# Performance work log

Hardware: AMD Instinct MI355X
Metric: run time of the kernel (lower is better)

Reference implementation:

```python
import jax, jax.numpy as jnp
import numpy as np

N = 4096


def setup_inputs() -> dict:
    key = jax.random.key(0)
    ks = jax.random.split(key, 5)
    s = 1.0 / np.sqrt(N)  # PyTorch Linear default init scale
    return {
        "outer": jax.random.normal(ks[0], (N, N), dtype=jnp.float32),
        "W_slice": jax.random.uniform(ks[1], (N, N), jnp.float32, -s, s),
        "b_slice": jax.random.uniform(ks[2], (N,), jnp.float32, -s, s),
        "W_q": jax.random.uniform(ks[3], (N, N), jnp.float32, -s, s),
        "b_q": jax.random.uniform(ks[4], (N,), jnp.float32, -s, s),
    }


def reference(outer, W_slice, b_slice, W_q, b_q):
    # k = sigmoid(Linear(outer)) then transposed: [n, n] -> [n, n]
    k = jax.nn.sigmoid(outer @ W_slice.T + b_slice).T
    # q = sigmoid(Linear(outer)): [n, n]
    q = jax.nn.sigmoid(outer @ W_q.T + b_q)
    # elementwise score, softmax over last dim (legacy nn.Softmax dim=1 for 2D)
    attn = jax.nn.softmax(q * k, axis=1)
    # weighted sum then reduce: [n, n] @ [n, n] -> [n, n] -> sum(-1) -> [n]
    out = (attn @ outer).sum(-1)
    return out
```

## Files before the change

### kernel.cpp

```cpp
#include <hip/hip_runtime.h>
#include <hip/hip_bf16.h>
#include <hip/hip_fp16.h>

#define NN 4096

typedef __attribute__((ext_vector_type(8))) __bf16 bf16x8;
typedef __attribute__((ext_vector_type(4))) float f32x4;
typedef __attribute__((ext_vector_type(8))) _Float16 f16x8;

static __device__ __forceinline__ unsigned short f2bf_bits(float x) {
  __hip_bfloat16 h = __float2bfloat16(x);
  return __builtin_bit_cast(unsigned short, h);
}

__global__ __launch_bounds__(256) void cast_rowsum_kernel(
    const float* __restrict__ in, __hip_bfloat16* __restrict__ ob,
    float* __restrict__ s) {
  const int row = blockIdx.x;
  const int t = threadIdx.x;
  const float4* rp = (const float4*)(in + (size_t)row * NN);
  unsigned short* op = (unsigned short*)(ob + (size_t)row * NN);
  float sum = 0.f;
#pragma unroll
  for (int it = 0; it < 4; ++it) {
    const int idx = it * 256 + t;
    float4 v = rp[idx];
    sum += (v.x + v.y) + (v.z + v.w);
    ushort4 b;
    b.x = f2bf_bits(v.x);
    b.y = f2bf_bits(v.y);
    b.z = f2bf_bits(v.z);
    b.w = f2bf_bits(v.w);
    *(ushort4*)(op + idx * 4) = b;
  }
#pragma unroll
  for (int o = 32; o > 0; o >>= 1) sum += __shfl_xor(sum, o);
  __shared__ float r[4];
  if ((t & 63) == 0) r[t >> 6] = sum;
  __syncthreads();
  if (t == 0) s[row] = (r[0] + r[1]) + (r[2] + r[3]);
}

__global__ __launch_bounds__(256) void cast_kernel(
    const float* __restrict__ in, __hip_bfloat16* __restrict__ ob) {
  const size_t idx = ((size_t)blockIdx.x * 256 + threadIdx.x) * 4;
  float4 v = *(const float4*)(in + idx);
  ushort4 b;
  b.x = f2bf_bits(v.x);
  b.y = f2bf_bits(v.y);
  b.z = f2bf_bits(v.z);
  b.w = f2bf_bits(v.w);
  *(ushort4*)((unsigned short*)ob + idx) = b;
}

#define BAR() asm volatile("s_barrier" ::: "memory")
#define VMW(N) asm volatile("s_waitcnt vmcnt(" #N ")" ::: "memory")
#define MFMA_(a, b, c) __builtin_amdgcn_mfma_f32_16x16x32_bf16((a), (b), (c), 0, 0, 0)
#define NOOP ((void)0)

#define STAGE_A(dbuf, g, ktE)                                                  \
  do {                                                                         \
    const int r0_ = wm * 128 + (g) * 32 + (wid & 3) * 8;                       \
    __builtin_amdgcn_global_load_lds(                                          \
        (const __attribute__((address_space(1))) void*)(Ag +                   \
            ((size_t)r0_ << 12) + (ktE) + lrowoff),                            \
        (__attribute__((address_space(3))) void*)(&As[dbuf][r0_ * 64]), 16, 0, \
        0);                                                                    \
  } while (0)

#define STAGE_B(dbuf, q, ktE)                                                  \
  do {                                                                         \
    const int r0_ = (q) * 64 + wid * 8;                                        \
    __builtin_amdgcn_global_load_lds(                                          \
        (const __attribute__((address_space(1))) void*)(Bg +                   \
            ((size_t)r0_ << 12) + (ktE) + lrowoff),                            \
        (__attribute__((address_space(3))) void*)(&Bs[dbuf][r0_ * 64]), 16, 0, \
        0);                                                                    \
  } while (0)

#define NOSA(a, b, c) ((void)0)
#define NOSB(a, b, c) ((void)0)

#define LDA8(cb, off) (*(const bf16x8*)((const char*)As[cb] + (off)))
#define LDB8(cb, off) (*(const bf16x8*)((const char*)Bs[cb] + (off)))

#define LOAD_A(cb, g)                                                          \
  af[0] = LDA8(cb, aoff0 + (2 * (g)) * 2048);                                  \
  af[1] = LDA8(cb, aoff1 + (2 * (g)) * 2048);                                  \
  af[2] = LDA8(cb, aoff0 + (2 * (g) + 1) * 2048);                              \
  af[3] = LDA8(cb, aoff1 + (2 * (g) + 1) * 2048);

#define MFMA_PH(g)                                                             \
  __builtin_amdgcn_s_setprio(1);                                               \
  acc[2 * (g)][0] = MFMA_(af[0], bfr[0][0], acc[2 * (g)][0]);                  \
  acc[2 * (g)][1] = MFMA_(af[0], bfr[1][0], acc[2 * (g)][1]);                  \
  acc[2 * (g)][2] = MFMA_(af[0], bfr[2][0], acc[2 * (g)][2]);                  \
  acc[2 * (g)][3] = MFMA_(af[0], bfr[3][0], acc[2 * (g)][3]);                  \
  acc[2 * (g) + 1][0] = MFMA_(af[2], bfr[0][0], acc[2 * (g) + 1][0]);          \
  acc[2 * (g) + 1][1] = MFMA_(af[2], bfr[1][0], acc[2 * (g) + 1][1]);          \
  acc[2 * (g) + 1][2] = MFMA_(af[2], bfr[2][0], acc[2 * (g) + 1][2]);          \
  acc[2 * (g) + 1][3] = MFMA_(af[2], bfr[3][0], acc[2 * (g) + 1][3]);          \
  acc[2 * (g)][0] = MFMA_(af[1], bfr[0][1], acc[2 * (g)][0]);                  \
  acc[2 * (g)][1] = MFMA_(af[1], bfr[1][1], acc[2 * (g)][1]);                  \
  acc[2 * (g)][2] = MFMA_(af[1], bfr[2][1], acc[2 * (g)][2]);                  \
  acc[2 * (g)][3] = MFMA_(af[1], bfr[3][1], acc[2 * (g)][3]);                  \
  acc[2 * (g) + 1][0] = MFMA_(af[3], bfr[0][1], acc[2 * (g) + 1][0]);          \
  acc[2 * (g) + 1][1] = MFMA_(af[3], bfr[1][1], acc[2 * (g) + 1][1]);          \
  acc[2 * (g) + 1][2] = MFMA_(af[3], bfr[2][1], acc[2 * (g) + 1][2]);          \
  acc[2 * (g) + 1][3] = MFMA_(af[3], bfr[3][1], acc[2 * (g) + 1][3]);          \
  __builtin_amdgcn_s_setprio(0);

#define KTILE(cb, kn1, kn2, SA, SB0, SBX, W0, W1, W2, W3)                      \
  {                                                                            \
    bfr[0][0] = LDB8(cb, boff0 + 0);                                           \
    bfr[0][1] = LDB8(cb, boff1 + 0);                                           \
    bfr[1][0] = LDB8(cb, boff0 + 2048);                                        \
    bfr[1][1] = LDB8(cb, boff1 + 2048);                                        \
    bfr[2][0] = LDB8(cb, boff0 + 4096);                                        \
    bfr[2][1] = LDB8(cb, boff1 + 4096);                                        \
    bfr[3][0] = LDB8(cb, boff0 + 6144);                                        \
    bfr[3][1] = LDB8(cb, boff1 + 6144);                                        \
    LOAD_A(cb, 0);                                                             \
    SA((cb) ^ 1, 0, kn1);                                                      \
    SB0;                                                                       \
    BAR();                                                                     \
    MFMA_PH(0);                                                                \
    W0;                                                                        \
    BAR();                                                                     \
    LOAD_A(cb, 1);                                                             \
    SA((cb) ^ 1, 1, kn1);                                                      \
    SBX(cb, 0, kn2);                                                           \
    BAR();                                                                     \
    MFMA_PH(1);                                                                \
    W1;                                                                        \
    BAR();                                                                     \
    LOAD_A(cb, 2);                                                             \
    SA((cb) ^ 1, 2, kn1);                                                      \
    SBX(cb, 1, kn2);                                                           \
    BAR();                                                                     \
    MFMA_PH(2);                                                                \
    W2;                                                                        \
    BAR();                                                                     \
    LOAD_A(cb, 3);                                                             \
    SA((cb) ^ 1, 3, kn1);                                                      \
    SBX(cb, 2, kn2);                                                           \
    BAR();                                                                     \
    MFMA_PH(3);                                                                \
    W3;                                                                        \
    BAR();                                                                     \
  }

__global__ __launch_bounds__(512, 2) void gemm_sig(
    const unsigned short* __restrict__ A, const unsigned short* __restrict__ B,
    const float* __restrict__ bias, __half* __restrict__ C, int bias_row) {
  __shared__ __align__(128) unsigned short As[2][16384];
  __shared__ __align__(128) unsigned short Bs[2][16384];

  const int tid = threadIdx.x;
  const int wid = tid >> 6;
  const int lane = tid & 63;
  const int wm = wid >> 2;
  const int wn = wid & 3;

  const int brow = blockIdx.x * 256;
  const int bcol = blockIdx.y * 256;

  const unsigned short* Ag = A + (size_t)brow * NN;
  const unsigned short* Bg = B + (size_t)bcol * NN;

  const size_t lrowoff = (size_t)(lane >> 3) * NN + (((lane & 7) ^ (lane >> 3)) * 8);

  const int fr = lane & 15;
  const int frlow = lane & 7;
  const int quad = lane >> 4;
  const int aoff0 = (wm * 128 + fr) * 128 + (((quad) ^ frlow) << 4);
  const int aoff1 = (wm * 128 + fr) * 128 + (((quad + 4) ^ frlow) << 4);
  const int boff0 = (wn * 64 + fr) * 128 + (((quad) ^ frlow) << 4);
  const int boff1 = (wn * 64 + fr) * 128 + (((quad + 4) ^ frlow) << 4);

  f32x4 acc[8][4];
#pragma unroll
  for (int m = 0; m < 8; ++m)
#pragma unroll
    for (int n = 0; n < 4; ++n) acc[m][n] = (f32x4){0.f, 0.f, 0.f, 0.f};

  bf16x8 bfr[4][2], af[4];

  STAGE_B(0, 0, 0);
  STAGE_B(0, 1, 0);
  STAGE_B(0, 2, 0);
  STAGE_B(0, 3, 0);
  STAGE_A(0, 0, 0);
  STAGE_A(0, 1, 0);
  STAGE_A(0, 2, 0);
  STAGE_A(0, 3, 0);
  STAGE_B(1, 0, 64);
  STAGE_B(1, 1, 64);
  STAGE_B(1, 2, 64);
  VMW(6);
  BAR();

  int kt = 0;
  for (int it = 0; it < 31; ++it) {
    const int k1 = kt + 64, k2 = kt + 128, k3 = kt + 192;
    KTILE(0, k1, k2, STAGE_A, STAGE_B(1, 3, k1), STAGE_B, VMW(6), VMW(6),
          VMW(6), VMW(6));
    KTILE(1, k2, k3, STAGE_A, STAGE_B(0, 3, k2), STAGE_B, VMW(6), VMW(6),
          VMW(6), VMW(6));
    kt += 128;
  }

  KTILE(0, 4032, 0, STAGE_A, STAGE_B(1, 3, 4032), NOSB, VMW(6), VMW(5), VMW(4),
        VMW(3));
  KTILE(1, 0, 0, NOSA, NOOP, NOSB, VMW(2), VMW(1), VMW(0), NOOP);

  const int cr0 = (lane >> 4) * 4;
  const int cc = lane & 15;
#pragma unroll
  for (int m = 0; m < 8; ++m) {
#pragma unroll
    for (int n = 0; n < 4; ++n) {
#pragma unroll
      for (int j = 0; j < 4; ++j) {
        const int gi = brow + wm * 128 + m * 16 + cr0 + j;
        const int gj = bcol + wn * 64 + n * 16 + cc;
        float v = acc[m][n][j] + (bias_row ? bias[gi] : bias[gj]);
        C[(size_t)gi * NN + gj] = __float2half(1.0f / (1.0f + __expf(-v)));
      }
    }
  }
}

__global__ __launch_bounds__(256) void softmax_out_kernel(
    const __half* __restrict__ q, const __half* __restrict__ k,
    const float* __restrict__ s, float* __restrict__ out) {
  const int i = blockIdx.x;
  const int t = threadIdx.x;
  const __half* qr = q + (size_t)i * NN;
  const __half* kr = k + (size_t)i * NN;
  float se = 0.f, ses = 0.f;
#pragma unroll
  for (int it = 0; it < 2; ++it) {
    const int j0 = (it * 256 + t) * 8;
    f16x8 qv = *(const f16x8*)(qr + j0);
    f16x8 kv = *(const f16x8*)(kr + j0);
    float4 s0 = *(const float4*)(s + j0);
    float4 s1 = *(const float4*)(s + j0 + 4);
    float sj[8] = {s0.x, s0.y, s0.z, s0.w, s1.x, s1.y, s1.z, s1.w};
#pragma unroll
    for (int u = 0; u < 8; ++u) {
      float sc = (float)qv[u] * (float)kv[u];
      float e = __expf(sc);
      se += e;
      ses += e * sj[u];
    }
  }
#pragma unroll
  for (int o = 32; o > 0; o >>= 1) {
    se += __shfl_xor(se, o);
    ses += __shfl_xor(ses, o);
  }
  __shared__ float r1[4], r2[4];
  if ((t & 63) == 0) {
    r1[t >> 6] = se;
    r2[t >> 6] = ses;
  }
  __syncthreads();
  if (t == 0)
    out[i] = ((r2[0] + r2[1]) + (r2[2] + r2[3])) /
             ((r1[0] + r1[1]) + (r1[2] + r1[3]));
}

extern "C" void kernel_launch(void* const* d_in, const int* in_sizes, int n_in,
                              void* d_out, int out_size, void* d_ws,
                              size_t ws_size, hipStream_t stream) {
  const float* outer = (const float*)d_in[0];
  const float* W_slice = (const float*)d_in[1];
  const float* b_slice = (const float*)d_in[2];
  const float* W_q = (const float*)d_in[3];
  const float* b_q = (const float*)d_in[4];
  float* out = (float*)d_out;

  char* ws = (char*)d_ws;
  const size_t MSZ = (size_t)NN * NN * 2;
  __hip_bfloat16* outer_bf = (__hip_bfloat16*)(ws);
  __hip_bfloat16* wsl_bf = (__hip_bfloat16*)(ws + MSZ);
  __hip_bfloat16* wq_bf = (__hip_bfloat16*)(ws + 2 * MSZ);
  __half* qh = (__half*)(ws + 3 * MSZ);
  __half* kh = (__half*)(ws + 4 * MSZ);
  float* s = (float*)(ws + 5 * MSZ);

  cast_rowsum_kernel<<<NN, 256, 0, stream>>>(outer, outer_bf, s);
  cast_kernel<<<NN * NN / 1024, 256, 0, stream>>>(W_slice, wsl_bf);
  cast_kernel<<<NN * NN / 1024, 256, 0, stream>>>(W_q, wq_bf);

  dim3 g(16, 16);
  gemm_sig<<<g, 512, 0, stream>>>((const unsigned short*)outer_bf,
                                  (const unsigned short*)wq_bf, b_q, qh, 0);
  gemm_sig<<<g, 512, 0, stream>>>((const unsigned short*)wsl_bf,
                                  (const unsigned short*)outer_bf, b_slice, kh,
                                  1);

  softmax_out_kernel<<<NN, 256, 0, stream>>>(qh, kh, s, out);
}
```

Baseline: 500.8 us.

## Restructure GEMM prefetch schedule and remap blocks to XCD-local tiles

Reorders the global-to-LDS staging inside each K tile so the two halves of the A tile and all four B chunks are issued in paired batches across phases. The per-phase vmcnt waits are collapsed into one wait at the end of the tile, which reduces stall points and deepens prefetch. The launch grid becomes 1D, and block IDs are remapped so that blocks dispatched to the same XCD cover a compact 4x8 region of output tiles, improving L2 reuse of A and B rows. This risks a correctness race if the buffer being staged into is still being read, and longer waits at the tile end.

```diff
diff --git a/kernel.cpp b/kernel.cpp
--- a/kernel.cpp
+++ b/kernel.cpp
@@ -110,7 +110,7 @@
   acc[2 * (g) + 1][3] = MFMA_(af[3], bfr[3][1], acc[2 * (g) + 1][3]);          \
   __builtin_amdgcn_s_setprio(0);
 
-#define KTILE(cb, kn1, kn2, SA, SB0, SBX, W0, W1, W2, W3)                      \
+#define KTILE(cb, kn1, kn2, SA0, SBX, SA3, W)                                  \
   {                                                                            \
     bfr[0][0] = LDB8(cb, boff0 + 0);                                           \
     bfr[0][1] = LDB8(cb, boff1 + 0);                                           \
@@ -121,32 +121,29 @@
     bfr[3][0] = LDB8(cb, boff0 + 6144);                                        \
     bfr[3][1] = LDB8(cb, boff1 + 6144);                                        \
     LOAD_A(cb, 0);                                                             \
-    SA((cb) ^ 1, 0, kn1);                                                      \
-    SB0;                                                                       \
+    SA0((cb) ^ 1, 2, kn1);                                                     \
+    SA0((cb) ^ 1, 3, kn1);                                                     \
     BAR();                                                                     \
     MFMA_PH(0);                                                                \
-    W0;                                                                        \
     BAR();                                                                     \
     LOAD_A(cb, 1);                                                             \
-    SA((cb) ^ 1, 1, kn1);                                                      \
     SBX(cb, 0, kn2);                                                           \
+    SBX(cb, 1, kn2);                                                           \
     BAR();                                                                     \
     MFMA_PH(1);                                                                \
-    W1;                                                                        \
     BAR();                                                                     \
     LOAD_A(cb, 2);                                                             \
-    SA((cb) ^ 1, 2, kn1);                                                      \
-    SBX(cb, 1, kn2);                                                           \
+    SBX(cb, 2, kn2);                                                           \
+    SBX(cb, 3, kn2);                                                           \
     BAR();                                                                     \
     MFMA_PH(2);                                                                \
-    W2;                                                                        \
     BAR();                                                                     \
     LOAD_A(cb, 3);                                                             \
-    SA((cb) ^ 1, 3, kn1);                                                      \
-    SBX(cb, 2, kn2);                                                           \
+    SA3(cb, 0, kn2);                                                           \
+    SA3(cb, 1, kn2);                                                           \
     BAR();                                                                     \
     MFMA_PH(3);                                                                \
-    W3;                                                                        \
+    W;                                                                         \
     BAR();                                                                     \
   }
 
@@ -162,8 +159,11 @@
   const int wm = wid >> 2;
   const int wn = wid & 3;
 
-  const int brow = blockIdx.x * 256;
-  const int bcol = blockIdx.y * 256;
+  const int bid = blockIdx.x;
+  const int xcd = bid & 7;
+  const int idx = bid >> 3;
+  const int brow = ((xcd >> 1) * 4 + (idx >> 3)) * 256;
+  const int bcol = ((xcd & 1) * 8 + (idx & 7)) * 256;
 
   const unsigned short* Ag = A + (size_t)brow * NN;
   const unsigned short* Bg = B + (size_t)bcol * NN;
@@ -197,22 +197,20 @@
   STAGE_B(1, 0, 64);
   STAGE_B(1, 1, 64);
   STAGE_B(1, 2, 64);
+  STAGE_B(1, 3, 64);
+  STAGE_A(1, 0, 64);
+  STAGE_A(1, 1, 64);
   VMW(6);
   BAR();
 
   int kt = 0;
   for (int it = 0; it < 31; ++it) {
-    const int k1 = kt + 64, k2 = kt + 128, k3 = kt + 192;
-    KTILE(0, k1, k2, STAGE_A, STAGE_B(1, 3, k1), STAGE_B, VMW(6), VMW(6),
-          VMW(6), VMW(6));
-    KTILE(1, k2, k3, STAGE_A, STAGE_B(0, 3, k2), STAGE_B, VMW(6), VMW(6),
-          VMW(6), VMW(6));
+    KTILE(0, kt + 64, kt + 128, STAGE_A, STAGE_B, STAGE_A, VMW(6));
+    KTILE(1, kt + 128, kt + 192, STAGE_A, STAGE_B, STAGE_A, VMW(6));
     kt += 128;
   }
-
-  KTILE(0, 4032, 0, STAGE_A, STAGE_B(1, 3, 4032), NOSB, VMW(6), VMW(5), VMW(4),
-        VMW(3));
-  KTILE(1, 0, 0, NOSA, NOOP, NOSB, VMW(2), VMW(1), VMW(0), NOOP);
+  KTILE(0, 4032, 0, STAGE_A, NOSB, NOSA, VMW(0));
+  KTILE(1, 0, 0, NOSA, NOSB, NOSA, NOOP);
 
   const int cr0 = (lane >> 4) * 4;
   const int cc = lane & 15;
@@ -294,12 +292,11 @@
   cast_kernel<<<NN * NN / 1024, 256, 0, stream>>>(W_slice, wsl_bf);
   cast_kernel<<<NN * NN / 1024, 256, 0, stream>>>(W_q, wq_bf);
 
-  dim3 g(16, 16);
-  gemm_sig<<<g, 512, 0, stream>>>((const unsigned short*)outer_bf,
-                                  (const unsigned short*)wq_bf, b_q, qh, 0);
-  gemm_sig<<<g, 512, 0, stream>>>((const unsigned short*)wsl_bf,
-                                  (const unsigned short*)outer_bf, b_slice, kh,
-                                  1);
+  gemm_sig<<<256, 512, 0, stream>>>((const unsigned short*)outer_bf,
+                                    (const unsigned short*)wq_bf, b_q, qh, 0);
+  gemm_sig<<<256, 512, 0, stream>>>((const unsigned short*)wsl_bf,
+                                    (const unsigned short*)outer_bf, b_slice,
+                                    kh, 1);
 
   softmax_out_kernel<<<NN, 256, 0, stream>>>(qh, kh, s, out);
 }
```

Measured after the change: 460.2 us. 1.09x faster.
